# Optimization experiments

Measured on AMD Instinct MI355X. Metric: run time of the kernel, lower is better.

The kernel has to match this reference:

```python
import jax, jax.numpy as jnp
import numpy as np

N = 100000      # num nodes
E = 3200000     # num edges (avg degree 32)
F = 512         # num_features
D = 256         # args.dim
C = 64          # num_classes
K = 10          # APPNP iterations
ALPHA = 0.1


def setup_inputs() -> dict:
    key = jax.random.key(0)
    ks = jax.random.split(key, 6)
    x = jax.random.normal(ks[0], (N, F), dtype=jnp.float32)
    edge_index = jax.random.randint(ks[1], (2, E), 0, N, dtype=jnp.int64)
    edge_weight_train = jax.random.normal(ks[2], (E,), dtype=jnp.float32)
    x_weight = jnp.ones((F,), dtype=jnp.float32)
    W1 = jax.random.normal(ks[3], (F, D), dtype=jnp.float32) * 0.02
    b1 = jnp.zeros((D,), dtype=jnp.float32)
    W2 = jax.random.normal(ks[4], (D, C), dtype=jnp.float32) * 0.02
    b2 = jnp.zeros((C,), dtype=jnp.float32)
    return {"x": x, "edge_index": edge_index, "edge_weight_train": edge_weight_train,
            "x_weight": x_weight, "W1": W1, "b1": b1, "W2": W2, "b2": b2}


def reference(x, edge_index, edge_weight_train, x_weight, W1, b1, W2, b2):
    row, col = edge_index[0], edge_index[1]
    # adj_sparse branch: mask edges with |w|==0, weight = sigmoid(w).
    # Filtering edges == zeroing their weight (degrees and messages scale by w).
    edge_mask = jnp.abs(edge_weight_train) > 0
    w = jnp.where(edge_mask, jax.nn.sigmoid(edge_weight_train), 0.0)
    # gcn_norm with self-loops (fill value 1.0)
    loop = jnp.arange(N, dtype=row.dtype)
    row2 = jnp.concatenate([row, loop])
    col2 = jnp.concatenate([col, loop])
    w2 = jnp.concatenate([w, jnp.ones((N,), dtype=w.dtype)])
    deg = jax.ops.segment_sum(w2, col2, num_segments=N)
    dinv = jnp.where(deg > 0, jax.lax.rsqrt(jnp.maximum(deg, 1e-12)), 0.0)
    norm = dinv[row2] * w2 * dinv[col2]  # [E+N]

    # feature_sparse branch
    x_mask = (jnp.abs(x_weight) > 0).astype(x.dtype)
    xw = jax.nn.sigmoid(x_weight) * x_mask
    xin = x * xw  # broadcast over nodes

    h = jax.nn.relu(xin @ W1 + b1)          # [N, D] (dropout is eval no-op)
    z0 = h @ W2 + b2                        # [N, C]

    z = z0
    for _ in range(K):
        msg = z[row2] * norm[:, None]       # gather + scale, [E+N, C]
        agg = jax.ops.segment_sum(msg, col2, num_segments=N)
        z = (1.0 - ALPHA) * agg + ALPHA * z0
    return jax.nn.log_softmax(z, axis=1)
```

## Files before the change

kernel.cpp:

```cpp
#include <hip/hip_runtime.h>
#include <hip/hip_bf16.h>
#include <cstdint>
#include <cstddef>

#define ALPHA 0.1f
#define K_ITERS 10
#define NPART 8

typedef __attribute__((ext_vector_type(8))) short bf16x8;
typedef __attribute__((ext_vector_type(4))) float f32x4;
typedef __attribute__((ext_vector_type(4))) unsigned int u32x4;

#define U15INV (1.0f / 32767.0f)

__device__ __forceinline__ unsigned short f2bf(float f) {
    unsigned int u = __float_as_uint(f);
    u += 0x7fffu + ((u >> 16) & 1u);
    return (unsigned short)(u >> 16);
}
__device__ __forceinline__ float bflo(unsigned int u) {
    return __uint_as_float(u << 16);
}
__device__ __forceinline__ float bfhi(unsigned int u) {
    return __uint_as_float(u & 0xffff0000u);
}
__device__ __forceinline__ unsigned int pack2(float a, float b) {
    return (unsigned int)f2bf(a) | ((unsigned int)f2bf(b) << 16);
}
__device__ __forceinline__ unsigned int u15q(float w) {
    return (unsigned int)(w * 32767.0f + 0.5f);
}
__device__ __forceinline__ int xcd_id() {
    unsigned int x;
    asm volatile("s_getreg_b32 %0, hwreg(20, 0, 32)" : "=s"(x));
    return (int)(x & (NPART - 1));
}


__global__ __launch_bounds__(256) void init_cnt_k(int* cntp, int* flag, int total) {
    int i = blockIdx.x * 256 + threadIdx.x;
    if (i == 0) *flag = 0;
    if (i < total) cntp[i] = 0;
}

__global__ __launch_bounds__(256) void zero_csr_k(unsigned int* cs, int total) {
    int i = blockIdx.x * 256 + threadIdx.x;
    if (i < total) cs[i] = 0;
}

__global__ void detect_idx_k(const void* ei, int* flag, int E_, int N_) {
    int tid = threadIdx.x;
    const long long* p = (const long long*)ei;
    int bad = 0;
    int lim = (E_ < 4096) ? E_ : 4096;
    for (int i = tid; i < lim; i += 256) {
        long long v = p[i];
        if (v < 0 || v >= (long long)N_) bad = 1;
    }
    if (bad) atomicOr(flag, 1);
}

__global__ __launch_bounds__(256) void prep_edges_k(const void* ei, const float* ew,
                                                    unsigned long long* epack, int* cntp,
                                                    const int* flag, int E_, int N_) {
    int e = blockIdx.x * 256 + threadIdx.x;
    if (e >= E_) return;
    int is32 = *flag;
    unsigned long long r, c;
    if (is32) {
        const int* p = (const int*)ei;
        r = (unsigned long long)(unsigned int)p[e];
        c = (unsigned long long)(unsigned int)p[(size_t)E_ + e];
    } else {
        const long long* p = (const long long*)ei;
        r = (unsigned long long)p[e];
        c = (unsigned long long)p[(size_t)E_ + e];
    }
    float t = ew[e];
    float wv = (fabsf(t) > 0.0f) ? 1.0f / (1.0f + expf(-t)) : 0.0f;
    unsigned long long part = (unsigned long long)xcd_id();
    unsigned long long rk = (unsigned long long)(unsigned int)
        __hip_atomic_fetch_add(&cntp[(size_t)part * N_ + (int)c], 1,
                               __ATOMIC_RELAXED, __HIP_MEMORY_SCOPE_WORKGROUP);
    epack[e] = r | (c << 17) | ((unsigned long long)u15q(wv) << 34)
                 | (part << 49) | (rk << 52);
}

__global__ __launch_bounds__(256) void combine_k(const int* cntp, int* pofs, int* cnt8, int N_) {
    int i = blockIdx.x * 256 + threadIdx.x;
    if (i >= N_) return;
    int s = 0;
    #pragma unroll
    for (int p = 0; p < NPART; ++p) {
        size_t idx = (size_t)p * N_ + i;
        int v = cntp[idx];
        pofs[idx] = s;
        s += v;
    }
    cnt8[i] = (s + 7) & ~7;
}

__global__ __launch_bounds__(256) void scan1_k(const int* cnt, int* bsum, int N_) {
    __shared__ int sm[256];
    int t = threadIdx.x, i = blockIdx.x * 256 + t;
    sm[t] = (i < N_) ? cnt[i] : 0;
    __syncthreads();
    for (int off = 128; off; off >>= 1) {
        if (t < off) sm[t] += sm[t + off];
        __syncthreads();
    }
    if (t == 0) bsum[blockIdx.x] = sm[0];
}

__global__ __launch_bounds__(1024) void scan2_k(const int* bsum, int* boff, int nb) {
    __shared__ int sm[1024];
    int t = threadIdx.x;
    int v = (t < nb) ? bsum[t] : 0;
    sm[t] = v;
    __syncthreads();
    for (int off = 1; off < 1024; off <<= 1) {
        int x = (t >= off) ? sm[t - off] : 0;
        __syncthreads();
        sm[t] += x;
        __syncthreads();
    }
    if (t < nb) boff[t] = sm[t] - v;
}

__global__ __launch_bounds__(256) void scan3_k(const int* cnt, const int* boff, int* rowstart, int N_) {
    __shared__ int sm[256];
    int t = threadIdx.x, i = blockIdx.x * 256 + t;
    int v = (i < N_) ? cnt[i] : 0;
    sm[t] = v;
    __syncthreads();
    for (int off = 1; off < 256; off <<= 1) {
        int x = (t >= off) ? sm[t - off] : 0;
        __syncthreads();
        sm[t] += x;
        __syncthreads();
    }
    if (i < N_)  rowstart[i]  = boff[blockIdx.x] + sm[t] - v;
    if (i == N_ - 1) rowstart[N_] = boff[blockIdx.x] + sm[t];
}

__global__ __launch_bounds__(256) void fill_csr_k(const unsigned long long* epack, const int* pofs,
                                                  const int* rowstart, unsigned int* cs,
                                                  int E_, int N_) {
    int e = blockIdx.x * 256 + threadIdx.x;
    if (e >= E_) return;
    unsigned long long v = epack[e];
    unsigned int r   = (unsigned int)(v & 0x1ffffu);
    int          c   = (int)((v >> 17) & 0x1ffffu);
    unsigned int w15 = (unsigned int)((v >> 34) & 0x7fffu);
    int         part = (int)((v >> 49) & 7u);
    int           rk = (int)(v >> 52);
    int pos = rowstart[c] + pofs[(size_t)part * N_ + c] + rk;
    cs[pos] = r | (w15 << 17);
}

__global__ __launch_bounds__(256) void deg_dinv_k(const unsigned int* __restrict__ cs,
                                                  const int* __restrict__ rowstart,
                                                  float* __restrict__ dinv, int N_) {
    int node = blockIdx.x * 8 + (threadIdx.x >> 5);
    int l = threadIdx.x & 31;
    if (node >= N_) return;
    int s = rowstart[node], e = rowstart[node + 1];
    float sum = 0.0f;
    for (int j = s + l; j < e; j += 32) sum += (float)(cs[j] >> 17) * U15INV;
    #pragma unroll
    for (int off = 16; off; off >>= 1) sum += __shfl_xor(sum, off, 64);
    float d = sum + 1.0f;
    if (l == 0) dinv[node] = (d > 0.0f) ? rsqrtf(fmaxf(d, 1e-12f)) : 0.0f;
}

__global__ __launch_bounds__(256) void norm_k(unsigned int* __restrict__ cs,
                                              const int* __restrict__ rowstart,
                                              const float* __restrict__ dinv, int N_) {
    int node = blockIdx.x * 8 + (threadIdx.x >> 5);
    int l = threadIdx.x & 31;
    if (node >= N_) return;
    int s = rowstart[node], e = rowstart[node + 1];
    float dc = dinv[node];
    for (int j = s + l; j < e; j += 32) {
        unsigned int v = cs[j];
        unsigned int src = v & 0x1ffffu;
        float w = (float)(v >> 17) * U15INV;
        float nm = dinv[src] * w * dc;
        cs[j] = src | (u15q(nm) << 17);
    }
}

__global__ __launch_bounds__(256) void w1t_k(const float* W1, const float* xw, unsigned short* W1bT, int F_, int D_) {
    int i = blockIdx.x * 256 + threadIdx.x;
    if (i >= F_ * D_) return;
    int k = i / D_, n = i % D_;
    float t = xw[k];
    float s = (fabsf(t) > 0.0f) ? 1.0f / (1.0f + expf(-t)) : 0.0f;
    W1bT[(size_t)n * F_ + k] = f2bf(W1[i] * s);
}

__global__ __launch_bounds__(256) void w2t_k(const float* W2, unsigned short* W2bT, int D_, int C_) {
    int i = blockIdx.x * 256 + threadIdx.x;
    if (i >= D_ * C_) return;
    int k = i / C_, n = i % C_;
    W2bT[(size_t)n * D_ + k] = f2bf(W2[i]);
}

template<int BN, bool A_BF16, bool RELU, bool OUT_BF16>
__global__ __launch_bounds__(256) void mfma_gemm_k(const void* __restrict__ Av,
                                                   const unsigned short* __restrict__ BT,
                                                   const float* __restrict__ bias,
                                                   void* __restrict__ Cout,
                                                   int M, int K, int Nn) {
    const int BK = 32;
    __shared__ __align__(16) unsigned short Asl[2][4][128][8];
    __shared__ __align__(16) unsigned short Bsl[2][4][BN][8];

    int tid = threadIdx.x;
    int row0 = blockIdx.x * 128;
    int n0 = blockIdx.y * BN;

    int wid = tid >> 6, lane = tid & 63;
    int wm = wid & 1, wn = wid >> 1;
    const int MT = 4;
    const int NT = BN / 32;
    int lrow = lane & 15, kg = lane >> 4;

    f32x4 acc[MT][NT];
    #pragma unroll
    for (int i = 0; i < MT; ++i)
        #pragma unroll
        for (int j = 0; j < NT; ++j) acc[i][j] = (f32x4){0.f, 0.f, 0.f, 0.f};

    int ar = tid >> 1;
    int akh = (tid & 1) * 16;
    int agrow = row0 + ar;
    bool avalid = agrow < M;

    int bn_ = tid >> 1;
    int bkh = (tid & 1) * 16;
    bool bvalid = bn_ < BN;

    float    fa[16];
    unsigned short ha[16];
    bf16x8   bv0, bv1;

    auto loadTile = [&](int k0) {
        if (A_BF16) {
            if (avalid) {
                const unsigned short* Ab = (const unsigned short*)Av;
                const bf16x8* p = (const bf16x8*)&Ab[(size_t)agrow * K + k0 + akh];
                *(bf16x8*)&ha[0] = p[0];
                *(bf16x8*)&ha[8] = p[1];
            }
        } else {
            if (avalid) {
                const float* Af = (const float*)Av;
                const f32x4* p = (const f32x4*)&Af[(size_t)agrow * K + k0 + akh];
                #pragma unroll
                for (int q = 0; q < 4; ++q) *(f32x4*)&fa[q * 4] = p[q];
            }
        }
        if (bvalid) {
            const bf16x8* p = (const bf16x8*)&BT[(size_t)(n0 + bn_) * K + k0 + bkh];
            bv0 = p[0]; bv1 = p[1];
        }
    };
    auto stageTile = [&](int buf) {
        unsigned short av[16];
        if (A_BF16) {
            #pragma unroll
            for (int q = 0; q < 16; ++q) av[q] = avalid ? ha[q] : (unsigned short)0;
        } else {
            #pragma unroll
            for (int q = 0; q < 16; ++q) av[q] = avalid ? f2bf(fa[q]) : (unsigned short)0;
        }
        *(bf16x8*)&Asl[buf][(akh >> 3) + 0][ar][0] = *(bf16x8*)&av[0];
        *(bf16x8*)&Asl[buf][(akh >> 3) + 1][ar][0] = *(bf16x8*)&av[8];
        if (bvalid) {
            *(bf16x8*)&Bsl[buf][(bkh >> 3) + 0][bn_][0] = bv0;
            *(bf16x8*)&Bsl[buf][(bkh >> 3) + 1][bn_][0] = bv1;
        }
    };

    int nsteps = K / BK;
    loadTile(0);
    stageTile(0);
    __syncthreads();

    int cur = 0;
    for (int step = 0; step < nsteps; ++step) {
        bool more = (step + 1) < nsteps;
        if (more) loadTile((step + 1) * BK);

        bf16x8 af[MT], bfr[NT];
        #pragma unroll
        for (int i = 0; i < MT; ++i)
            af[i] = *(bf16x8*)&Asl[cur][kg][wm * 64 + i * 16 + lrow][0];
        #pragma unroll
        for (int j = 0; j < NT; ++j)
            bfr[j] = *(bf16x8*)&Bsl[cur][kg][wn * (BN / 2) + j * 16 + lrow][0];
        #pragma unroll
        for (int i = 0; i < MT; ++i)
            #pragma unroll
            for (int j = 0; j < NT; ++j)
                acc[i][j] = __builtin_amdgcn_mfma_f32_16x16x32_bf16(af[i], bfr[j], acc[i][j], 0, 0, 0);

        if (more) stageTile(cur ^ 1);
        __syncthreads();
        cur ^= 1;
    }

    #pragma unroll
    for (int i = 0; i < MT; ++i) {
        #pragma unroll
        for (int j = 0; j < NT; ++j) {
            int col = n0 + wn * (BN / 2) + j * 16 + lrow;
            float bv = bias[col];
            #pragma unroll
            for (int r = 0; r < 4; ++r) {
                int grow = row0 + wm * 64 + i * 16 + kg * 4 + r;
                if (grow < M) {
                    float v = acc[i][j][r] + bv;
                    if (RELU) v = fmaxf(v, 0.0f);
                    if (OUT_BF16) ((unsigned short*)Cout)[(size_t)grow * Nn + col] = f2bf(v);
                    else          ((float*)Cout)[(size_t)grow * Nn + col] = v;
                }
            }
        }
    }
}

template<bool LAST>
__global__ __launch_bounds__(256) void prop8_k(const unsigned short* __restrict__ z,
                                               const unsigned short* __restrict__ z0,
                                               const int* __restrict__ rowstart,
                                               const unsigned int* __restrict__ cs,
                                               const float* __restrict__ dinv,
                                               unsigned short* __restrict__ znew,
                                               float* __restrict__ out, int N_) {
    int node = blockIdx.x * 32 + (threadIdx.x >> 3);
    int l = threadIdx.x & 7;
    if (node >= N_) return;
    int s = rowstart[node], e = rowstart[node + 1];
    float d = dinv[node];
    size_t ro = (size_t)node * 64 + l * 8;
    u32x4 zs = *(const u32x4*)&z[ro];
    float dd = d * d;
    float a[8];
    a[0] = dd * bflo(zs.x); a[1] = dd * bfhi(zs.x);
    a[2] = dd * bflo(zs.y); a[3] = dd * bfhi(zs.y);
    a[4] = dd * bflo(zs.z); a[5] = dd * bfhi(zs.z);
    a[6] = dd * bflo(zs.w); a[7] = dd * bfhi(zs.w);

    for (int j = s; j < e; j += 8) {
        u32x4 p0 = __builtin_nontemporal_load((const u32x4*)&cs[j]);
        u32x4 p1 = __builtin_nontemporal_load((const u32x4*)&cs[j + 4]);
        unsigned int pe[8] = { p0.x, p0.y, p0.z, p0.w, p1.x, p1.y, p1.z, p1.w };
        u32x4 g[8];
        #pragma unroll
        for (int q = 0; q < 8; ++q)
            g[q] = *(const u32x4*)&z[(size_t)(pe[q] & 0x1ffffu) * 64 + l * 8];
        #pragma unroll
        for (int q = 0; q < 8; ++q) {
            float w = (float)(pe[q] >> 17) * U15INV;
            a[0] += w * bflo(g[q].x); a[1] += w * bfhi(g[q].x);
            a[2] += w * bflo(g[q].y); a[3] += w * bfhi(g[q].y);
            a[4] += w * bflo(g[q].z); a[5] += w * bfhi(g[q].z);
            a[6] += w * bflo(g[q].w); a[7] += w * bfhi(g[q].w);
        }
    }

    u32x4 z0v = *(const u32x4*)&z0[ro];
    float v[8];
    float z0f[8] = { bflo(z0v.x), bfhi(z0v.x), bflo(z0v.y), bfhi(z0v.y),
                     bflo(z0v.z), bfhi(z0v.z), bflo(z0v.w), bfhi(z0v.w) };
    #pragma unroll
    for (int q = 0; q < 8; ++q) v[q] = (1.0f - ALPHA) * a[q] + ALPHA * z0f[q];

    if (!LAST) {
        u32x4 o;
        o.x = pack2(v[0], v[1]); o.y = pack2(v[2], v[3]);
        o.z = pack2(v[4], v[5]); o.w = pack2(v[6], v[7]);
        __builtin_nontemporal_store(o, (u32x4*)&znew[ro]);
    } else {
        float m = v[0];
        #pragma unroll
        for (int q = 1; q < 8; ++q) m = fmaxf(m, v[q]);
        #pragma unroll
        for (int off = 1; off < 8; off <<= 1) m = fmaxf(m, __shfl_xor(m, off, 64));
        float sum = 0.0f;
        #pragma unroll
        for (int q = 0; q < 8; ++q) sum += expf(v[q] - m);
        #pragma unroll
        for (int off = 1; off < 8; off <<= 1) sum += __shfl_xor(sum, off, 64);
        float lg = logf(sum);
        float4 o0 = make_float4(v[0] - m - lg, v[1] - m - lg, v[2] - m - lg, v[3] - m - lg);
        float4 o1 = make_float4(v[4] - m - lg, v[5] - m - lg, v[6] - m - lg, v[7] - m - lg);
        *(float4*)&out[ro] = o0;
        *(float4*)&out[ro + 4] = o1;
    }
}


extern "C" void kernel_launch(void* const* d_in, const int* in_sizes, int n_in,
                              void* d_out, int out_size, void* d_ws, size_t ws_size,
                              hipStream_t stream) {
    const float* x   = (const float*)d_in[0];
    const void*  ei  = d_in[1];
    const float* ew  = (const float*)d_in[2];
    const float* xw  = (const float*)d_in[3];
    const float* W1  = (const float*)d_in[4];
    const float* b1  = (const float*)d_in[5];
    const float* W2  = (const float*)d_in[6];
    const float* b2  = (const float*)d_in[7];

    const int F_ = in_sizes[3];
    const int N_ = in_sizes[0] / F_;
    const int E_ = in_sizes[2];
    const int D_ = in_sizes[5];
    const int C_ = in_sizes[7];

    const int E8 = E_ + 7 * N_;

    char* base = (char*)d_ws;
    size_t off = 0;
    auto take = [&](size_t bytes) -> void* {
        void* p = base + off;
        off += (bytes + 255) & ~(size_t)255;
        return p;
    };
    unsigned long long* epack = (unsigned long long*)take((size_t)E_ * 8);
    unsigned int* cs = (unsigned int*)take((size_t)E8 * 4);
    int*   cntp     = (int*)  take((size_t)NPART * N_ * 4);
    int*   pofs     = (int*)  take((size_t)NPART * N_ * 4);
    int*   cnt8     = (int*)  take((size_t)N_ * 4);
    float* dinv     = (float*)take((size_t)N_ * 4);
    int*   rowstart = (int*)  take((size_t)(N_ + 1) * 4);
    int*   flag     = (int*)  take(256);
    int*   bsum     = (int*)  take(4096 * 4);
    int*   boff     = (int*)  take(4096 * 4);
    unsigned short* W1bT = (unsigned short*)take((size_t)F_ * D_ * 2);
    unsigned short* W2bT = (unsigned short*)take((size_t)D_ * C_ * 2);
    unsigned short* h    = (unsigned short*)take((size_t)N_ * D_ * 2);
    unsigned short* z0b  = (unsigned short*)take((size_t)N_ * C_ * 2);
    unsigned short* za   = (unsigned short*)take((size_t)N_ * C_ * 2);
    unsigned short* zb   = (unsigned short*)take((size_t)N_ * C_ * 2);

    (void)ws_size; (void)n_in; (void)out_size;

    int nblk = (N_ + 255) / 256;
    int eblk = (E_ + 255) / 256;

    init_cnt_k<<<((size_t)NPART * N_ + 255) / 256, 256, 0, stream>>>(cntp, flag, NPART * N_);
    zero_csr_k<<<(E8 + 255) / 256, 256, 0, stream>>>(cs, E8);
    detect_idx_k<<<1, 256, 0, stream>>>(ei, flag, E_, N_);
    prep_edges_k<<<eblk, 256, 0, stream>>>(ei, ew, epack, cntp, flag, E_, N_);
    combine_k<<<nblk, 256, 0, stream>>>(cntp, pofs, cnt8, N_);
    scan1_k<<<nblk, 256, 0, stream>>>(cnt8, bsum, N_);
    scan2_k<<<1, 1024, 0, stream>>>(bsum, boff, nblk);
    scan3_k<<<nblk, 256, 0, stream>>>(cnt8, boff, rowstart, N_);
    fill_csr_k<<<eblk, 256, 0, stream>>>(epack, pofs, rowstart, cs, E_, N_);
    int gblk8 = (N_ + 7) / 8;
    deg_dinv_k<<<gblk8, 256, 0, stream>>>(cs, rowstart, dinv, N_);
    norm_k<<<gblk8, 256, 0, stream>>>(cs, rowstart, dinv, N_);
    w1t_k<<<(F_ * D_ + 255) / 256, 256, 0, stream>>>(W1, xw, W1bT, F_, D_);
    w2t_k<<<(D_ * C_ + 255) / 256, 256, 0, stream>>>(W2, W2bT, D_, C_);

    int gx = (N_ + 127) / 128;
    mfma_gemm_k<128, false, true, true><<<dim3(gx, D_ / 128), 256, 0, stream>>>(
        (const void*)x, W1bT, b1, (void*)h, N_, F_, D_);
    mfma_gemm_k<64, true, false, true><<<dim3(gx, C_ / 64), 256, 0, stream>>>(
        (const void*)h, W2bT, b2, (void*)z0b, N_, D_, C_);

    int pblk = (N_ + 31) / 32;
    const unsigned short* cur = z0b;
    unsigned short* bufs[2] = { za, zb };
    for (int it = 0; it < K_ITERS - 1; ++it) {
        unsigned short* dst = bufs[it & 1];
        prop8_k<false><<<pblk, 256, 0, stream>>>(cur, z0b, rowstart, cs, dinv, dst, nullptr, N_);
        cur = dst;
    }
    prop8_k<true><<<pblk, 256, 0, stream>>>(cur, z0b, rowstart, cs, dinv, nullptr, (float*)d_out, N_);
}
```

Measured before the change: 930.2 us.

## Widen first GEMM to full 256 columns per block, merge init kernels

The first GEMM now uses 512-thread blocks, each covering all 256 output columns. Each row tile of the fp32 input x is therefore read and converted to bf16 once instead of twice across two column blocks. The two zeroing kernels are merged into one launch, and the second GEMM is specialised without templates. The propagation kernel now loads z0 with nontemporal hints and uses ordinary stores for z, which changes how the z0 and z buffers behave in cache. The larger block raises LDS use and register pressure per block.

```diff
diff --git a/kernel.cpp b/kernel.cpp
--- a/kernel.cpp
+++ b/kernel.cpp
@@ -37,15 +37,12 @@
 }
 
 
-__global__ __launch_bounds__(256) void init_cnt_k(int* cntp, int* flag, int total) {
+__global__ __launch_bounds__(256) void setup_k(int* cntp, unsigned int* cs, int* flag,
+                                               int ncnt, int ncs) {
     int i = blockIdx.x * 256 + threadIdx.x;
     if (i == 0) *flag = 0;
-    if (i < total) cntp[i] = 0;
-}
-
-__global__ __launch_bounds__(256) void zero_csr_k(unsigned int* cs, int total) {
-    int i = blockIdx.x * 256 + threadIdx.x;
-    if (i < total) cs[i] = 0;
+    if (i < ncnt) cntp[i] = 0;
+    if (i < ncs) cs[i] = 0;
 }
 
 __global__ void detect_idx_k(const void* ei, int* flag, int E_, int N_) {
@@ -206,75 +203,145 @@
     W2bT[(size_t)n * D_ + k] = f2bf(W2[i]);
 }
 
-template<int BN, bool A_BF16, bool RELU, bool OUT_BF16>
-__global__ __launch_bounds__(256) void mfma_gemm_k(const void* __restrict__ Av,
+__global__ __launch_bounds__(512) void gemm1_512_k(const float* __restrict__ A,
                                                    const unsigned short* __restrict__ BT,
                                                    const float* __restrict__ bias,
-                                                   void* __restrict__ Cout,
+                                                   unsigned short* __restrict__ C,
                                                    int M, int K, int Nn) {
     const int BK = 32;
     __shared__ __align__(16) unsigned short Asl[2][4][128][8];
-    __shared__ __align__(16) unsigned short Bsl[2][4][BN][8];
+    __shared__ __align__(16) unsigned short Bsl[2][4][256][8];
 
     int tid = threadIdx.x;
     int row0 = blockIdx.x * 128;
-    int n0 = blockIdx.y * BN;
-
     int wid = tid >> 6, lane = tid & 63;
     int wm = wid & 1, wn = wid >> 1;
-    const int MT = 4;
+    int lrow = lane & 15, kg = lane >> 4;
+
+    f32x4 acc[4][4];
+    #pragma unroll
+    for (int i = 0; i < 4; ++i)
+        #pragma unroll
+        for (int j = 0; j < 4; ++j) acc[i][j] = (f32x4){0.f, 0.f, 0.f, 0.f};
+
+    int ar = tid >> 2, akg = tid & 3;
+    int agrow = row0 + ar;
+    bool avalid = agrow < M;
+    int bn_ = tid >> 1, bkh = (tid & 1) * 16;
+
+    float fa[8];
+    bf16x8 bv0, bv1;
+
+    auto loadTile = [&](int k0) {
+        if (avalid) {
+            const f32x4* p = (const f32x4*)&A[(size_t)agrow * K + k0 + akg * 8];
+            *(f32x4*)&fa[0] = p[0];
+            *(f32x4*)&fa[4] = p[1];
+        }
+        const bf16x8* p = (const bf16x8*)&BT[(size_t)bn_ * K + k0 + bkh];
+        bv0 = p[0]; bv1 = p[1];
+    };
+    auto stageTile = [&](int buf) {
+        unsigned short av[8];
+        #pragma unroll
+        for (int q = 0; q < 8; ++q) av[q] = avalid ? f2bf(fa[q]) : (unsigned short)0;
+        *(bf16x8*)&Asl[buf][akg][ar][0] = *(bf16x8*)&av[0];
+        *(bf16x8*)&Bsl[buf][(bkh >> 3) + 0][bn_][0] = bv0;
+        *(bf16x8*)&Bsl[buf][(bkh >> 3) + 1][bn_][0] = bv1;
+    };
+
+    int nsteps = K / BK;
+    loadTile(0);
+    stageTile(0);
+    __syncthreads();
+
+    int cur = 0;
+    for (int step = 0; step < nsteps; ++step) {
+        bool more = (step + 1) < nsteps;
+        if (more) loadTile((step + 1) * BK);
+
+        bf16x8 af[4], bfr[4];
+        #pragma unroll
+        for (int i = 0; i < 4; ++i)
+            af[i] = *(bf16x8*)&Asl[cur][kg][wm * 64 + i * 16 + lrow][0];
+        #pragma unroll
+        for (int j = 0; j < 4; ++j)
+            bfr[j] = *(bf16x8*)&Bsl[cur][kg][wn * 64 + j * 16 + lrow][0];
+        #pragma unroll
+        for (int i = 0; i < 4; ++i)
+            #pragma unroll
+            for (int j = 0; j < 4; ++j)
+                acc[i][j] = __builtin_amdgcn_mfma_f32_16x16x32_bf16(af[i], bfr[j], acc[i][j], 0, 0, 0);
+
+        if (more) stageTile(cur ^ 1);
+        __syncthreads();
+        cur ^= 1;
+    }
+
+    #pragma unroll
+    for (int i = 0; i < 4; ++i) {
+        #pragma unroll
+        for (int j = 0; j < 4; ++j) {
+            int col = wn * 64 + j * 16 + lrow;
+            float bv = bias[col];
+            #pragma unroll
+            for (int r = 0; r < 4; ++r) {
+                int grow = row0 + wm * 64 + i * 16 + kg * 4 + r;
+                if (grow < M) {
+                    float v = fmaxf(acc[i][j][r] + bv, 0.0f);
+                    C[(size_t)grow * Nn + col] = f2bf(v);
+                }
+            }
+        }
+    }
+}
+
+__global__ __launch_bounds__(256) void gemm2_k(const unsigned short* __restrict__ Ab,
+                                               const unsigned short* __restrict__ BT,
+                                               const float* __restrict__ bias,
+                                               unsigned short* __restrict__ C,
+                                               int M, int K, int Nn) {
+    const int BN = 64, BK = 32;
+    __shared__ __align__(16) unsigned short Asl[2][4][128][8];
+    __shared__ __align__(16) unsigned short Bsl[2][4][BN][8];
+
+    int tid = threadIdx.x;
+    int row0 = blockIdx.x * 128;
+    int wid = tid >> 6, lane = tid & 63;
+    int wm = wid & 1, wn = wid >> 1;
     const int NT = BN / 32;
     int lrow = lane & 15, kg = lane >> 4;
 
-    f32x4 acc[MT][NT];
-    #pragma unroll
-    for (int i = 0; i < MT; ++i)
+    f32x4 acc[4][NT];
+    #pragma unroll
+    for (int i = 0; i < 4; ++i)
         #pragma unroll
         for (int j = 0; j < NT; ++j) acc[i][j] = (f32x4){0.f, 0.f, 0.f, 0.f};
 
-    int ar = tid >> 1;
-    int akh = (tid & 1) * 16;
+    int ar = tid >> 1, akh = (tid & 1) * 16;
     int agrow = row0 + ar;
     bool avalid = agrow < M;
-
-    int bn_ = tid >> 1;
-    int bkh = (tid & 1) * 16;
+    int bn_ = tid >> 1, bkh = (tid & 1) * 16;
     bool bvalid = bn_ < BN;
 
-    float    fa[16];
     unsigned short ha[16];
-    bf16x8   bv0, bv1;
+    bf16x8 bv0, bv1;
 
     auto loadTile = [&](int k0) {
-        if (A_BF16) {
-            if (avalid) {
-                const unsigned short* Ab = (const unsigned short*)Av;
-                const bf16x8* p = (const bf16x8*)&Ab[(size_t)agrow * K + k0 + akh];
-                *(bf16x8*)&ha[0] = p[0];
-                *(bf16x8*)&ha[8] = p[1];
-            }
-        } else {
-            if (avalid) {
-                const float* Af = (const float*)Av;
-                const f32x4* p = (const f32x4*)&Af[(size_t)agrow * K + k0 + akh];
-                #pragma unroll
-                for (int q = 0; q < 4; ++q) *(f32x4*)&fa[q * 4] = p[q];
-            }
+        if (avalid) {
+            const bf16x8* p = (const bf16x8*)&Ab[(size_t)agrow * K + k0 + akh];
+            *(bf16x8*)&ha[0] = p[0];
+            *(bf16x8*)&ha[8] = p[1];
         }
         if (bvalid) {
-            const bf16x8* p = (const bf16x8*)&BT[(size_t)(n0 + bn_) * K + k0 + bkh];
+            const bf16x8* p = (const bf16x8*)&BT[(size_t)bn_ * K + k0 + bkh];
             bv0 = p[0]; bv1 = p[1];
         }
     };
     auto stageTile = [&](int buf) {
         unsigned short av[16];
-        if (A_BF16) {
-            #pragma unroll
-            for (int q = 0; q < 16; ++q) av[q] = avalid ? ha[q] : (unsigned short)0;
-        } else {
-            #pragma unroll
-            for (int q = 0; q < 16; ++q) av[q] = avalid ? f2bf(fa[q]) : (unsigned short)0;
-        }
+        #pragma unroll
+        for (int q = 0; q < 16; ++q) av[q] = avalid ? ha[q] : (unsigned short)0;
         *(bf16x8*)&Asl[buf][(akh >> 3) + 0][ar][0] = *(bf16x8*)&av[0];
         *(bf16x8*)&Asl[buf][(akh >> 3) + 1][ar][0] = *(bf16x8*)&av[8];
         if (bvalid) {
@@ -293,15 +360,15 @@
         bool more = (step + 1) < nsteps;
         if (more) loadTile((step + 1) * BK);
 
-        bf16x8 af[MT], bfr[NT];
-        #pragma unroll
-        for (int i = 0; i < MT; ++i)
+        bf16x8 af[4], bfr[NT];
+        #pragma unroll
+        for (int i = 0; i < 4; ++i)
             af[i] = *(bf16x8*)&Asl[cur][kg][wm * 64 + i * 16 + lrow][0];
         #pragma unroll
         for (int j = 0; j < NT; ++j)
             bfr[j] = *(bf16x8*)&Bsl[cur][kg][wn * (BN / 2) + j * 16 + lrow][0];
         #pragma unroll
-        for (int i = 0; i < MT; ++i)
+        for (int i = 0; i < 4; ++i)
             #pragma unroll
             for (int j = 0; j < NT; ++j)
                 acc[i][j] = __builtin_amdgcn_mfma_f32_16x16x32_bf16(af[i], bfr[j], acc[i][j], 0, 0, 0);
@@ -312,20 +379,16 @@
     }
 
     #pragma unroll
-    for (int i = 0; i < MT; ++i) {
+    for (int i = 0; i < 4; ++i) {
         #pragma unroll
         for (int j = 0; j < NT; ++j) {
-            int col = n0 + wn * (BN / 2) + j * 16 + lrow;
+            int col = wn * (BN / 2) + j * 16 + lrow;
             float bv = bias[col];
             #pragma unroll
             for (int r = 0; r < 4; ++r) {
                 int grow = row0 + wm * 64 + i * 16 + kg * 4 + r;
-                if (grow < M) {
-                    float v = acc[i][j][r] + bv;
-                    if (RELU) v = fmaxf(v, 0.0f);
-                    if (OUT_BF16) ((unsigned short*)Cout)[(size_t)grow * Nn + col] = f2bf(v);
-                    else          ((float*)Cout)[(size_t)grow * Nn + col] = v;
-                }
+                if (grow < M)
+                    C[(size_t)grow * Nn + col] = f2bf(acc[i][j][r] + bv);
             }
         }
     }
@@ -371,7 +434,7 @@
         }
     }
 
-    u32x4 z0v = *(const u32x4*)&z0[ro];
+    u32x4 z0v = __builtin_nontemporal_load((const u32x4*)&z0[ro]);
     float v[8];
     float z0f[8] = { bflo(z0v.x), bfhi(z0v.x), bflo(z0v.y), bfhi(z0v.y),
                      bflo(z0v.z), bfhi(z0v.z), bflo(z0v.w), bfhi(z0v.w) };
@@ -382,7 +445,7 @@
         u32x4 o;
         o.x = pack2(v[0], v[1]); o.y = pack2(v[2], v[3]);
         o.z = pack2(v[4], v[5]); o.w = pack2(v[6], v[7]);
-        __builtin_nontemporal_store(o, (u32x4*)&znew[ro]);
+        *(u32x4*)&znew[ro] = o;
     } else {
         float m = v[0];
         #pragma unroll
@@ -451,9 +514,10 @@
 
     int nblk = (N_ + 255) / 256;
     int eblk = (E_ + 255) / 256;
-
-    init_cnt_k<<<((size_t)NPART * N_ + 255) / 256, 256, 0, stream>>>(cntp, flag, NPART * N_);
-    zero_csr_k<<<(E8 + 255) / 256, 256, 0, stream>>>(cs, E8);
+    int ncnt = NPART * N_;
+    int setup_blk = ((ncnt > E8 ? ncnt : E8) + 255) / 256;
+
+    setup_k<<<setup_blk, 256, 0, stream>>>(cntp, cs, flag, ncnt, E8);
     detect_idx_k<<<1, 256, 0, stream>>>(ei, flag, E_, N_);
     prep_edges_k<<<eblk, 256, 0, stream>>>(ei, ew, epack, cntp, flag, E_, N_);
     combine_k<<<nblk, 256, 0, stream>>>(cntp, pofs, cnt8, N_);
@@ -468,10 +532,8 @@
     w2t_k<<<(D_ * C_ + 255) / 256, 256, 0, stream>>>(W2, W2bT, D_, C_);
 
     int gx = (N_ + 127) / 128;
-    mfma_gemm_k<128, false, true, true><<<dim3(gx, D_ / 128), 256, 0, stream>>>(
-        (const void*)x, W1bT, b1, (void*)h, N_, F_, D_);
-    mfma_gemm_k<64, true, false, true><<<dim3(gx, C_ / 64), 256, 0, stream>>>(
-        (const void*)h, W2bT, b2, (void*)z0b, N_, D_, C_);
+    gemm1_512_k<<<gx, 512, 0, stream>>>(x, W1bT, b1, h, N_, F_, D_);
+    gemm2_k<<<gx, 256, 0, stream>>>(h, W2bT, b2, z0b, N_, D_, C_);
 
     int pblk = (N_ + 31) / 32;
     const unsigned short* cur = z0b;
```

After: 896.5 us. 1.04x faster.
